# Performance work log

Measured on AMD Instinct MI355X. Metric: run time of the kernel, lower is better.

Reference implementation:

```python
import jax, jax.numpy as jnp
import numpy as np
from jax import lax

DIM = 128          # embedding dim
LG = 3             # layer_gnn
LC = 3             # layer_cnn
LO = 2             # layer_output
WIN = 11           # window -> conv kernel 23x23, padding 11 (SAME)
NF = 10000         # n_fingerprint
NW = 10000         # n_word
NA = 4096          # n_atoms
NWORDS = 16384     # protein length


def setup_inputs() -> dict:
    key = jax.random.key(0)
    ks = jax.random.split(key, 16)
    s = 1.0 / np.sqrt(DIM)
    s2 = 1.0 / np.sqrt(2 * DIM)
    K = 2 * WIN + 1
    return {
        "fingerprints": jax.random.randint(ks[0], (NA,), 0, NF),
        # sparse-ish binary adjacency like a molecular graph, scaled up
        "adjacency": (jax.random.uniform(ks[1], (NA, NA)) < 0.005).astype(jnp.float32),
        "words": jax.random.randint(ks[2], (NWORDS,), 0, NW),
        "emb_fp": jax.random.normal(ks[3], (NF, DIM), dtype=jnp.float32) * 0.1,
        "emb_word": jax.random.normal(ks[4], (NW, DIM), dtype=jnp.float32) * 0.1,
        "W_gnn_w": jax.random.normal(ks[5], (LG, DIM, DIM), dtype=jnp.float32) * s,
        "W_gnn_b": jax.random.normal(ks[6], (LG, DIM), dtype=jnp.float32) * s,
        "conv_w": jax.random.normal(ks[7], (LC, 1, 1, K, K), dtype=jnp.float32) * 0.02,
        "conv_b": jax.random.normal(ks[8], (LC, 1), dtype=jnp.float32) * 0.02,
        "W_att_w": jax.random.normal(ks[9], (DIM, DIM), dtype=jnp.float32) * s,
        "W_att_b": jax.random.normal(ks[10], (DIM,), dtype=jnp.float32) * s,
        "W_out_w": jax.random.normal(ks[11], (LO, 2 * DIM, 2 * DIM), dtype=jnp.float32) * s2,
        "W_out_b": jax.random.normal(ks[12], (LO, 2 * DIM), dtype=jnp.float32) * s2,
        "W_int_w": jax.random.normal(ks[13], (1, 2 * DIM), dtype=jnp.float32) * s2,
        "W_int_b": jax.random.normal(ks[14], (1,), dtype=jnp.float32) * s2,
    }


def _linear(x, w, b):
    # torch nn.Linear: y = x @ w.T + b
    return x @ w.T + b


def reference(fingerprints, adjacency, words, emb_fp, emb_word,
              W_gnn_w, W_gnn_b, conv_w, conv_b, W_att_w, W_att_b,
              W_out_w, W_out_b, W_int_w, W_int_b):
    # ---- Compound vector with GNN ----
    xs = emb_fp[fingerprints]                      # [NA, DIM]
    for l in range(LG):
        hs = jax.nn.relu(_linear(xs, W_gnn_w[l], W_gnn_b[l]))
        xs = xs + adjacency @ hs                   # residual message passing
    compound = jnp.mean(xs, axis=0, keepdims=True) # [1, DIM]

    # ---- Protein vector with attention-CNN ----
    ws = emb_word[words]                           # [NWORDS, DIM]
    img = ws[None, None]                           # [1, 1, NWORDS, DIM]
    for l in range(LC):
        img = lax.conv_general_dilated(
            img, conv_w[l], window_strides=(1, 1), padding='SAME',
            dimension_numbers=('NCHW', 'OIHW', 'NCHW'))
        img = img + conv_b[l].reshape(1, -1, 1, 1)
        img = jax.nn.leaky_relu(img, negative_slope=0.01)
    ws = img[0, 0]                                 # [NWORDS, DIM]

    h = jax.nn.relu(_linear(compound, W_att_w, W_att_b))   # [1, DIM]
    hs = jax.nn.relu(_linear(ws, W_att_w, W_att_b))        # [NWORDS, DIM]
    weights = jnp.tanh(h @ hs.T)                            # [1, NWORDS]
    ys = weights.T * hs                                     # [NWORDS, DIM]
    protein = jnp.mean(ys, axis=0, keepdims=True)           # [1, DIM]

    # ---- Concatenate and output ----
    cat = jnp.concatenate((compound, protein), axis=1)      # [1, 2*DIM]
    for l in range(LO):
        cat = jax.nn.relu(_linear(cat, W_out_w[l], W_out_b[l]))
    interaction = _linear(cat, W_int_w, W_int_b)            # [1, 1]
    return interaction
```

## Files before the change

### kernel.cpp

```cpp
#include <hip/hip_runtime.h>

#define DIM 128
#define NA 4096
#define NWORDS 16384
#define MAXNZ 256
#define KW 23
#define PAD 11

__global__ void k_gather(float* __restrict__ out, const float* __restrict__ tab,
                         const int* __restrict__ idx) {
  int t = blockIdx.x * blockDim.x + threadIdx.x;
  int r = t >> 5, c = t & 31;
  ((float4*)out)[t] = ((const float4*)(tab + (size_t)idx[r] * DIM))[c];
}

__global__ void k_adj_scan(int* __restrict__ cnt, int* __restrict__ colx,
                           float* __restrict__ valx, const float* __restrict__ adj) {
  int w = threadIdx.x >> 6, lane = threadIdx.x & 63;
  int row = blockIdx.x * 4 + w;
  const float4* ar = (const float4*)(adj + (size_t)row * NA);
  int count = 0;
  unsigned long long ltm = (1ull << lane) - 1ull;
  for (int c4 = lane; c4 < NA / 4; c4 += 64) {
    float4 v = ar[c4];
    #pragma unroll
    for (int e = 0; e < 4; ++e) {
      float ve = e == 0 ? v.x : e == 1 ? v.y : e == 2 ? v.z : v.w;
      unsigned long long m = __ballot(ve != 0.0f);
      if (ve != 0.0f) {
        int off = count + (int)__popcll(m & ltm);
        if (off < MAXNZ) { colx[row * MAXNZ + off] = c4 * 4 + e; valx[row * MAXNZ + off] = ve; }
      }
      count += (int)__popcll(m);
    }
  }
  if (lane == 0) cnt[row] = count;
}

__global__ __launch_bounds__(256) void k_linear_relu(
    float* __restrict__ out, const float* __restrict__ A,
    const float* __restrict__ W, const float* __restrict__ bias) {
  __shared__ float As[64 * 132];
  __shared__ float Ws[64 * 132];
  int mt = blockIdx.x >> 1, nt = blockIdx.x & 1;
  int r0 = mt * 64, c0 = nt * 64;
  int tid = threadIdx.x;
  for (int q = tid; q < 64 * 32; q += 256) {
    int row = q >> 5, c4 = q & 31;
    *(float4*)&As[row * 132 + c4 * 4] = *(const float4*)&A[(size_t)(r0 + row) * DIM + c4 * 4];
    *(float4*)&Ws[row * 132 + c4 * 4] = *(const float4*)&W[(size_t)(c0 + row) * DIM + c4 * 4];
  }
  __syncthreads();
  int rgr = tid & 15, cgr = tid >> 4;
  float acc[4][4] = {};
  #pragma unroll 4
  for (int k4 = 0; k4 < 32; ++k4) {
    int kk = ((k4 + rgr) & 31) * 4;
    float4 a[4], w[4];
    #pragma unroll
    for (int i = 0; i < 4; ++i) a[i] = *(const float4*)&As[(rgr * 4 + i) * 132 + kk];
    #pragma unroll
    for (int j = 0; j < 4; ++j) w[j] = *(const float4*)&Ws[(cgr * 4 + j) * 132 + kk];
    #pragma unroll
    for (int i = 0; i < 4; ++i)
      #pragma unroll
      for (int j = 0; j < 4; ++j)
        acc[i][j] += a[i].x * w[j].x + a[i].y * w[j].y + a[i].z * w[j].z + a[i].w * w[j].w;
  }
  #pragma unroll
  for (int i = 0; i < 4; ++i) {
    int r = r0 + rgr * 4 + i;
    int c = c0 + cgr * 4;
    float4 bv = *(const float4*)&bias[c];
    float4 o;
    o.x = acc[i][0] + bv.x; o.y = acc[i][1] + bv.y;
    o.z = acc[i][2] + bv.z; o.w = acc[i][3] + bv.w;
    o.x = o.x > 0.f ? o.x : 0.f; o.y = o.y > 0.f ? o.y : 0.f;
    o.z = o.z > 0.f ? o.z : 0.f; o.w = o.w > 0.f ? o.w : 0.f;
    *(float4*)&out[(size_t)r * DIM + c] = o;
  }
}

__global__ void k_spmm(float* __restrict__ xs, const float* __restrict__ hs,
                       const int* __restrict__ cnt, const int* __restrict__ colx,
                       const float* __restrict__ valx, const float* __restrict__ adj) {
  __shared__ int scol[MAXNZ];
  __shared__ float sval[MAXNZ];
  int r = blockIdx.x, d = threadIdx.x;
  int n = cnt[r];
  int m = (n <= MAXNZ) ? n : 0;
  for (int i = d; i < m; i += 128) {
    scol[i] = colx[r * MAXNZ + i];
    sval[i] = valx[r * MAXNZ + i];
  }
  __syncthreads();
  float acc = xs[(size_t)r * DIM + d];
  if (n <= MAXNZ) {
    for (int i = 0; i < n; ++i)
      acc += sval[i] * hs[(size_t)scol[i] * DIM + d];
  } else {
    for (int c = 0; c < NA; ++c) {
      float a = adj[(size_t)r * NA + c];
      if (a != 0.f) acc += a * hs[(size_t)c * DIM + d];
    }
  }
  xs[(size_t)r * DIM + d] = acc;
}

__global__ void k_mean(float* __restrict__ out, const float* __restrict__ in,
                       int rows_per_block, float scale) {
  __shared__ float red[256];
  int d = threadIdx.x & 127, half = threadIdx.x >> 7;
  int r0 = blockIdx.x * rows_per_block;
  float acc = 0.f;
  for (int r = r0 + half; r < r0 + rows_per_block; r += 2)
    acc += in[(size_t)r * DIM + d];
  red[threadIdx.x] = acc;
  __syncthreads();
  if (half == 0) atomicAdd(&out[d], (acc + red[threadIdx.x + 128]) * scale);
}

#define CROWS 32
#define TROWS 54
#define TCOLS 150
#define TSTR  164
__global__ __launch_bounds__(256) void k_conv(
    float* __restrict__ out, const float* __restrict__ in,
    const float* __restrict__ cw, const float* __restrict__ cb) {
  __shared__ float tile[TROWS * TSTR];
  int r0 = blockIdx.x * CROWS;
  int tid = threadIdx.x;
  for (int p = tid; p < TROWS * TCOLS; p += 256) {
    int rr = p / TCOLS, cc = p - rr * TCOLS;
    int gr = r0 - PAD + rr, gc = cc - PAD;
    float v = 0.f;
    if ((unsigned)gr < NWORDS && (unsigned)gc < DIM) v = in[(size_t)gr * DIM + gc];
    tile[rr * TSTR + cc] = v;
  }
  __syncthreads();
  int rl = tid & 31, cg = tid >> 5;
  int c0 = cg * 16;
  float acc[16] = {};
  float bias = cb[0];
  for (int dy = 0; dy < KW; ++dy) {
    const float* trow = &tile[(rl + dy) * TSTR + c0];
    float v[40];
    #pragma unroll
    for (int q = 0; q < 10; ++q) {
      float4 t4 = *(const float4*)&trow[q * 4];
      v[q * 4 + 0] = t4.x; v[q * 4 + 1] = t4.y;
      v[q * 4 + 2] = t4.z; v[q * 4 + 3] = t4.w;
    }
    const float* wr = cw + dy * KW;
    #pragma unroll
    for (int dx = 0; dx < KW; ++dx) {
      float wv = wr[dx];
      #pragma unroll
      for (int i = 0; i < 16; ++i) acc[i] += wv * v[i + dx];
    }
  }
  size_t ob = (size_t)(r0 + rl) * DIM + c0;
  #pragma unroll
  for (int q = 0; q < 4; ++q) {
    float4 o;
    float x0 = acc[q*4+0] + bias, x1 = acc[q*4+1] + bias;
    float x2 = acc[q*4+2] + bias, x3 = acc[q*4+3] + bias;
    o.x = x0 > 0.f ? x0 : 0.01f * x0;
    o.y = x1 > 0.f ? x1 : 0.01f * x1;
    o.z = x2 > 0.f ? x2 : 0.01f * x2;
    o.w = x3 > 0.f ? x3 : 0.01f * x3;
    *(float4*)&out[ob + q * 4] = o;
  }
}

__global__ void k_h(float* __restrict__ h, const float* __restrict__ comp,
                    const float* __restrict__ W, const float* __restrict__ b) {
  __shared__ float c[DIM];
  int j = threadIdx.x;
  c[j] = comp[j];
  __syncthreads();
  float acc = b[j];
  #pragma unroll
  for (int k4 = 0; k4 < 32; ++k4) {
    float4 w4 = *(const float4*)&W[j * DIM + k4 * 4];
    acc += c[k4*4+0] * w4.x + c[k4*4+1] * w4.y + c[k4*4+2] * w4.z + c[k4*4+3] * w4.w;
  }
  h[j] = acc > 0.f ? acc : 0.f;
}

__global__ __launch_bounds__(256) void k_attprot(
    float* __restrict__ prot, const float* __restrict__ hsA, const float* __restrict__ h) {
  __shared__ float lw[128];
  __shared__ float red[256];
  int tid = threadIdx.x;
  int w = tid >> 6, lane = tid & 63;
  int r0 = blockIdx.x * 128;
  float2 hv = ((const float2*)h)[lane];
  for (int rr = w; rr < 128; rr += 4) {
    float2 xv = ((const float2*)(hsA + (size_t)(r0 + rr) * DIM))[lane];
    float dt = hv.x * xv.x + hv.y * xv.y;
    for (int o = 32; o > 0; o >>= 1) dt += __shfl_xor(dt, o);
    if (lane == 0) lw[rr] = tanhf(dt);
  }
  __syncthreads();
  int d = tid & 127, half = tid >> 7;
  float acc = 0.f;
  for (int rr = half; rr < 128; rr += 2)
    acc += lw[rr] * hsA[(size_t)(r0 + rr) * DIM + d];
  red[tid] = acc;
  __syncthreads();
  if (half == 0) atomicAdd(&prot[d], (acc + red[tid + 128]) * (1.f / NWORDS));
}

__global__ __launch_bounds__(256) void k_final(
    float* __restrict__ out, const float* __restrict__ comp, const float* __restrict__ prot,
    const float* __restrict__ Wo, const float* __restrict__ bo,
    const float* __restrict__ Wi, const float* __restrict__ bi) {
  __shared__ float cat[256];
  __shared__ float wred[4];
  int t = threadIdx.x;
  int w = t >> 6, lane = t & 63;
  cat[t] = t < 128 ? comp[t] : prot[t - 128];
  __syncthreads();
  for (int l = 0; l < 2; ++l) {
    const float* Wl = Wo + l * 256 * 256;
    float acc = bo[l * 256 + t];
    #pragma unroll 8
    for (int k4 = 0; k4 < 64; ++k4) {
      float4 w4 = *(const float4*)&Wl[t * 256 + k4 * 4];
      acc += cat[k4*4+0] * w4.x + cat[k4*4+1] * w4.y + cat[k4*4+2] * w4.z + cat[k4*4+3] * w4.w;
    }
    __syncthreads();
    cat[t] = acc > 0.f ? acc : 0.f;
    __syncthreads();
  }
  float r = cat[t] * Wi[t];
  for (int o = 32; o > 0; o >>= 1) r += __shfl_xor(r, o);
  if (lane == 0) wred[w] = r;
  __syncthreads();
  if (t == 0) out[0] = wred[0] + wred[1] + wred[2] + wred[3] + bi[0];
}

extern "C" void kernel_launch(void* const* d_in, const int* in_sizes, int n_in,
                              void* d_out, int out_size, void* d_ws, size_t ws_size,
                              hipStream_t stream) {
  const int*   fingerprints = (const int*)d_in[0];
  const float* adjacency    = (const float*)d_in[1];
  const int*   words        = (const int*)d_in[2];
  const float* emb_fp       = (const float*)d_in[3];
  const float* emb_word     = (const float*)d_in[4];
  const float* W_gnn_w      = (const float*)d_in[5];
  const float* W_gnn_b      = (const float*)d_in[6];
  const float* conv_w       = (const float*)d_in[7];
  const float* conv_b       = (const float*)d_in[8];
  const float* W_att_w      = (const float*)d_in[9];
  const float* W_att_b      = (const float*)d_in[10];
  const float* W_out_w      = (const float*)d_in[11];
  const float* W_out_b      = (const float*)d_in[12];
  const float* W_int_w      = (const float*)d_in[13];
  const float* W_int_b      = (const float*)d_in[14];
  float* out = (float*)d_out;

  float* xs   = (float*)d_ws;
  float* hsb  = xs   + 524288;
  float* valx = hsb  + 524288;
  float* pa   = valx + 1048576;
  float* pb   = pa   + 2097152;
  float* hsA  = pb   + 2097152;
  float* attw = hsA  + 2097152;
  float* small= attw + 16384;
  int*   colx = (int*)(small + 512);
  int*   cntv = colx + 1048576;
  float* comp = small, *prot = small + 128, *hvec = small + 256;
  (void)attw;

  hipMemsetAsync(small, 0, 512 * sizeof(float), stream);

  k_gather<<<512, 256, 0, stream>>>(xs, emb_fp, fingerprints);
  k_adj_scan<<<1024, 256, 0, stream>>>(cntv, colx, valx, adjacency);
  for (int l = 0; l < 3; ++l) {
    k_linear_relu<<<128, 256, 0, stream>>>(hsb, xs, W_gnn_w + l * DIM * DIM, W_gnn_b + l * DIM);
    k_spmm<<<NA, 128, 0, stream>>>(xs, hsb, cntv, colx, valx, adjacency);
  }
  k_mean<<<32, 256, 0, stream>>>(comp, xs, 128, 1.0f / NA);

  k_gather<<<2048, 256, 0, stream>>>(pa, emb_word, words);
  k_conv<<<512, 256, 0, stream>>>(pb, pa, conv_w + 0 * 529, conv_b + 0);
  k_conv<<<512, 256, 0, stream>>>(pa, pb, conv_w + 1 * 529, conv_b + 1);
  k_conv<<<512, 256, 0, stream>>>(pb, pa, conv_w + 2 * 529, conv_b + 2);

  k_linear_relu<<<512, 256, 0, stream>>>(hsA, pb, W_att_w, W_att_b);
  k_h<<<1, 128, 0, stream>>>(hvec, comp, W_att_w, W_att_b);
  k_attprot<<<128, 256, 0, stream>>>(prot, hsA, hvec);

  k_final<<<1, 256, 0, stream>>>(out, comp, prot, W_out_w, W_out_b, W_int_w, W_int_b);
}
```

Baseline: 384.0 us.

## Remap conv threads to column-per-thread and fuse h computation into attprot

The 23x23 conv now gives each thread one column and 16 consecutive rows, and the loops are swapped so the outer loop runs over dx and a vertical strip of 38 values is reused across dy. The shared tile stride drops to 150. The separate single-block k_h kernel is removed; every attprot block recomputes the attention query vector from the compound vector, which saves a launch but repeats a 128x128 matvec per block. The new layout trades the old float4 shared loads for scalar loads, and output stores become scalar but coalesced across threads.

```diff
diff --git a/kernel.cpp b/kernel.cpp
--- a/kernel.cpp
+++ b/kernel.cpp
@@ -123,7 +123,7 @@
 #define CROWS 32
 #define TROWS 54
 #define TCOLS 150
-#define TSTR  164
+#define TSTR  150
 __global__ __launch_bounds__(256) void k_conv(
     float* __restrict__ out, const float* __restrict__ in,
     const float* __restrict__ cw, const float* __restrict__ cb) {
@@ -138,64 +138,54 @@
     tile[rr * TSTR + cc] = v;
   }
   __syncthreads();
-  int rl = tid & 31, cg = tid >> 5;
-  int c0 = cg * 16;
+  int col = tid & 127, rb = tid >> 7;
+  int rbase = rb * 16;
   float acc[16] = {};
+  for (int dx = 0; dx < KW; ++dx) {
+    float v[38];
+    #pragma unroll
+    for (int j = 0; j < 38; ++j)
+      v[j] = tile[(rbase + j) * TSTR + col + dx];
+    const float* wp = cw + dx;
+    #pragma unroll
+    for (int dy = 0; dy < KW; ++dy) {
+      float wv = wp[dy * KW];
+      #pragma unroll
+      for (int i = 0; i < 16; ++i) acc[i] += wv * v[i + dy];
+    }
+  }
   float bias = cb[0];
-  for (int dy = 0; dy < KW; ++dy) {
-    const float* trow = &tile[(rl + dy) * TSTR + c0];
-    float v[40];
-    #pragma unroll
-    for (int q = 0; q < 10; ++q) {
-      float4 t4 = *(const float4*)&trow[q * 4];
-      v[q * 4 + 0] = t4.x; v[q * 4 + 1] = t4.y;
-      v[q * 4 + 2] = t4.z; v[q * 4 + 3] = t4.w;
-    }
-    const float* wr = cw + dy * KW;
-    #pragma unroll
-    for (int dx = 0; dx < KW; ++dx) {
-      float wv = wr[dx];
-      #pragma unroll
-      for (int i = 0; i < 16; ++i) acc[i] += wv * v[i + dx];
-    }
-  }
-  size_t ob = (size_t)(r0 + rl) * DIM + c0;
   #pragma unroll
-  for (int q = 0; q < 4; ++q) {
-    float4 o;
-    float x0 = acc[q*4+0] + bias, x1 = acc[q*4+1] + bias;
-    float x2 = acc[q*4+2] + bias, x3 = acc[q*4+3] + bias;
-    o.x = x0 > 0.f ? x0 : 0.01f * x0;
-    o.y = x1 > 0.f ? x1 : 0.01f * x1;
-    o.z = x2 > 0.f ? x2 : 0.01f * x2;
-    o.w = x3 > 0.f ? x3 : 0.01f * x3;
-    *(float4*)&out[ob + q * 4] = o;
-  }
-}
-
-__global__ void k_h(float* __restrict__ h, const float* __restrict__ comp,
-                    const float* __restrict__ W, const float* __restrict__ b) {
-  __shared__ float c[DIM];
-  int j = threadIdx.x;
-  c[j] = comp[j];
-  __syncthreads();
-  float acc = b[j];
-  #pragma unroll
-  for (int k4 = 0; k4 < 32; ++k4) {
-    float4 w4 = *(const float4*)&W[j * DIM + k4 * 4];
-    acc += c[k4*4+0] * w4.x + c[k4*4+1] * w4.y + c[k4*4+2] * w4.z + c[k4*4+3] * w4.w;
-  }
-  h[j] = acc > 0.f ? acc : 0.f;
+  for (int i = 0; i < 16; ++i) {
+    float x = acc[i] + bias;
+    out[(size_t)(r0 + rbase + i) * DIM + col] = x > 0.f ? x : 0.01f * x;
+  }
 }
 
 __global__ __launch_bounds__(256) void k_attprot(
-    float* __restrict__ prot, const float* __restrict__ hsA, const float* __restrict__ h) {
+    float* __restrict__ prot, const float* __restrict__ hsA,
+    const float* __restrict__ comp, const float* __restrict__ W,
+    const float* __restrict__ b) {
+  __shared__ float cvec[DIM];
+  __shared__ float hv_s[DIM];
   __shared__ float lw[128];
   __shared__ float red[256];
   int tid = threadIdx.x;
   int w = tid >> 6, lane = tid & 63;
+  if (tid < 128) cvec[tid] = comp[tid];
+  __syncthreads();
+  if (tid < 128) {
+    float acc = b[tid];
+    #pragma unroll
+    for (int k4 = 0; k4 < 32; ++k4) {
+      float4 w4 = *(const float4*)&W[tid * DIM + k4 * 4];
+      acc += cvec[k4*4+0] * w4.x + cvec[k4*4+1] * w4.y + cvec[k4*4+2] * w4.z + cvec[k4*4+3] * w4.w;
+    }
+    hv_s[tid] = acc > 0.f ? acc : 0.f;
+  }
+  __syncthreads();
   int r0 = blockIdx.x * 128;
-  float2 hv = ((const float2*)h)[lane];
+  float2 hv = ((const float2*)hv_s)[lane];
   for (int rr = w; rr < 128; rr += 4) {
     float2 xv = ((const float2*)(hsA + (size_t)(r0 + rr) * DIM))[lane];
     float dt = hv.x * xv.x + hv.y * xv.y;
@@ -271,7 +261,7 @@
   float* small= attw + 16384;
   int*   colx = (int*)(small + 512);
   int*   cntv = colx + 1048576;
-  float* comp = small, *prot = small + 128, *hvec = small + 256;
+  float* comp = small, *prot = small + 128;
   (void)attw;
 
   hipMemsetAsync(small, 0, 512 * sizeof(float), stream);
@@ -290,8 +280,7 @@
   k_conv<<<512, 256, 0, stream>>>(pb, pa, conv_w + 2 * 529, conv_b + 2);
 
   k_linear_relu<<<512, 256, 0, stream>>>(hsA, pb, W_att_w, W_att_b);
-  k_h<<<1, 128, 0, stream>>>(hvec, comp, W_att_w, W_att_b);
-  k_attprot<<<128, 256, 0, stream>>>(prot, hsA, hvec);
+  k_attprot<<<128, 256, 0, stream>>>(prot, hsA, comp, W_att_w, W_att_b);
 
   k_final<<<1, 256, 0, stream>>>(out, comp, prot, W_out_w, W_out_b, W_int_w, W_int_b);
 }
```

Result: no change. 384.7 us (+0.2%).
